# Performance work log

Hardware: AMD Instinct MI355X
Metric: run time of the kernel (lower is better)

The kernel has to match this reference:

```python
import jax, jax.numpy as jnp
import numpy as np

B, C, H, W = 16, 512, 64, 64
HEADS = 8
DIL = 2  # dilation of the 3x3 depthwise conv (padding == dilation -> shape preserving)


def setup_inputs() -> dict:
    key = jax.random.key(0)
    ks = jax.random.split(key, 4)
    x = jax.random.normal(ks[0], (B, C, H, W), jnp.float32)
    # kaiming-normal-ish scales (fan_out, relu)
    w_qkv = jax.random.normal(ks[1], (3 * C, C), jnp.float32) * (2.0 / C) ** 0.5  # 1x1 conv weight
    w_dw = jax.random.normal(ks[2], (C, 3, 3), jnp.float32) * (2.0 / 9.0) ** 0.5  # depthwise 3x3
    w_out = jax.random.normal(ks[3], (C, C), jnp.float32) * (2.0 / C) ** 0.5      # 1x1 conv weight
    temperature = jnp.sqrt(jnp.asarray(C // HEADS, jnp.float32))                  # init sqrt(dim_per_head)
    return {"x": x, "w_qkv": w_qkv, "w_dw": w_dw, "w_out": w_out, "temperature": temperature}


def _dw_conv(y, w_dw):
    # depthwise dilated 3x3 conv, padding=dilation -> same spatial size
    rhs = w_dw[:, None, :, :]  # [C,1,3,3]
    return jax.lax.conv_general_dilated(
        y, rhs, window_strides=(1, 1), padding=((DIL, DIL), (DIL, DIL)),
        rhs_dilation=(DIL, DIL), feature_group_count=y.shape[1],
        dimension_numbers=("NCHW", "OIHW", "NCHW"))


def reference(x, w_qkv, w_dw, w_out, temperature):
    b, c, h, w = x.shape
    n = h * w
    d = c // HEADS
    # 1x1 qkv projection (bias-free conv == einsum)
    qkv = jnp.einsum("oc,bchw->bohw", w_qkv, x)  # [B,3C,H,W]
    q, k, v = jnp.split(qkv, 3, axis=1)
    # same depthwise conv applied to q,k,v: fold into batch, conv once
    qkv3 = _dw_conv(jnp.concatenate([q, k, v], axis=0), w_dw)  # [3B,C,H,W]
    q, k, v = jnp.split(qkv3, 3, axis=0)
    q = q.reshape(b, HEADS, d, n)
    k = k.reshape(b, HEADS, d, n)
    v = v.reshape(b, HEADS, d, n)
    # L2 normalize along the per-head channel dim (dim=2), eps=1e-12 like F.normalize
    l2 = lambda t: t / jnp.maximum(jnp.linalg.norm(t, axis=2, keepdims=True), 1e-12)
    q = l2(q)
    k = l2(k)
    # cross-covariance attention: [B,heads,d,d]
    attn = jnp.einsum("bhdn,bhen->bhde", q, k) / jnp.maximum(temperature, 1e-5)
    attn = jax.nn.softmax(attn, axis=-1)
    # dropout is identity in eval mode
    out = jnp.einsum("bhde,bhen->bhdn", attn, v).reshape(b, c, h, w)
    return jnp.einsum("oc,bchw->bohw", w_out, out)
```

## Files before the change

kernel.cpp:

```cpp
#include <hip/hip_runtime.h>

typedef __attribute__((ext_vector_type(8))) short bf16x8;
typedef __attribute__((ext_vector_type(8))) unsigned short ushort8;
typedef __attribute__((ext_vector_type(4))) float f32x4;
typedef __attribute__((ext_vector_type(4))) unsigned int u32x4;
typedef __attribute__((ext_vector_type(2))) unsigned int u32x2;

__device__ __forceinline__ float bf2f(unsigned short u) {
  union { unsigned int i; float f; } v; v.i = ((unsigned int)u) << 16; return v.f;
}
__device__ __forceinline__ float asf(unsigned int u) {
  union { unsigned int i; float f; } v; v.i = u; return v.f;
}
__device__ __forceinline__ unsigned short f2bf(float f) {
  union { float f; unsigned int i; } v; v.f = f;
  unsigned int u = v.i;
  return (unsigned short)((u + 0x7FFFu + ((u >> 16) & 1u)) >> 16);
}
__device__ __forceinline__ void gload16(const void* g, void* l) {
  __builtin_amdgcn_global_load_lds(
      (const __attribute__((address_space(1))) void*)g,
      (__attribute__((address_space(3))) void*)l, 16, 0, 0);
}

__global__ __launch_bounds__(256) void cvt_f32_bf16(const float* __restrict__ s,
                                                    unsigned short* __restrict__ d, int n) {
  int i = blockIdx.x * 256 + threadIdx.x;
  if (i < n) d[i] = f2bf(s[i]);
}

__global__ __launch_bounds__(256) void transpose_x(const float* __restrict__ x,
                                                   unsigned short* __restrict__ xt) {
  __shared__ float tile[64][65];
  const int b = blockIdx.z, ct = blockIdx.y, nt = blockIdx.x;
  const int t = threadIdx.x;
  const int r0 = t >> 6, col = t & 63;
  const float* src = x + ((size_t)b * 512 + ct * 64) * 4096 + nt * 64;
#pragma unroll
  for (int i = 0; i < 16; ++i) {
    int r = i * 4 + r0;
    tile[r][col] = src[(size_t)r * 4096 + col];
  }
  __syncthreads();
  unsigned short* dst = xt + ((size_t)b * 4096 + nt * 64) * 512 + ct * 64;
#pragma unroll
  for (int i = 0; i < 16; ++i) {
    int n = i * 4 + r0;
    dst[(size_t)n * 512 + col] = f2bf(tile[col][n]);
  }
}

__global__ __launch_bounds__(512, 2) void gemm_qkv_256(const unsigned short* __restrict__ A,
                                                       const unsigned short* __restrict__ B,
                                                       unsigned short* __restrict__ C) {
  __shared__ unsigned short lA[2][256 * 64];
  __shared__ unsigned short lB[2][256 * 64];
  const int gx = gridDim.x;
  const int nwg = gx * gridDim.y;
  int flat = blockIdx.x + gx * blockIdx.y;
  flat = (flat & 7) * (nwg >> 3) + (flat >> 3);
  const int bx = flat % gx;
  const int by = flat / gx;
  const size_t m0 = (size_t)by * 256;
  const size_t n0 = (size_t)bx * 256;

  const int t = threadIdx.x;
  const int lane = t & 63;
  const int wid = t >> 6;
  const int wm = wid >> 2, wn = wid & 3;
  const int ro = lane & 15, kq = lane >> 4;

  const int srow = t >> 3;
  const int kslot = (t & 7) ^ (srow & 7);
  const unsigned short* ga = A + (m0 + srow) * 512 + kslot * 8;
  const unsigned short* gb = B + (n0 + srow) * 512 + kslot * 8;

  f32x4 acc[8][4] = {};

  auto stage = [&](int kt, int bbuf) {
    char* da = (char*)(&lA[bbuf][0]) + t * 16;
    char* db = (char*)(&lB[bbuf][0]) + t * 16;
    const unsigned short* pa = ga + kt * 64;
    const unsigned short* pb = gb + kt * 64;
#pragma unroll
    for (int l = 0; l < 4; ++l) {
      gload16(pa + (size_t)(l * 64) * 512, da + l * 8192);
      gload16(pb + (size_t)(l * 64) * 512, db + l * 8192);
    }
  };

  stage(0, 0);
  __syncthreads();
  int buf = 0;
  for (int kt = 0; kt < 8; ++kt) {
    if (kt + 1 < 8) stage(kt + 1, buf ^ 1);
    const unsigned short* pa = &lA[buf][0];
    const unsigned short* pb = &lB[buf][0];
#pragma unroll
    for (int kk = 0; kk < 2; ++kk) {
      const int slot = ((kk << 2) | kq) ^ (ro & 7);
      bf16x8 a_[8], b_[4];
#pragma unroll
      for (int i = 0; i < 8; ++i) {
        const int row = wm * 128 + i * 16 + ro;
        a_[i] = *(const bf16x8*)&pa[row * 64 + slot * 8];
      }
#pragma unroll
      for (int j = 0; j < 4; ++j) {
        const int row = wn * 64 + j * 16 + ro;
        b_[j] = *(const bf16x8*)&pb[row * 64 + slot * 8];
      }
#pragma unroll
      for (int i = 0; i < 8; ++i)
#pragma unroll
        for (int j = 0; j < 4; ++j)
          acc[i][j] = __builtin_amdgcn_mfma_f32_16x16x32_bf16(a_[i], b_[j], acc[i][j], 0, 0, 0);
    }
    __syncthreads();
    buf ^= 1;
  }

#pragma unroll
  for (int i = 0; i < 8; ++i)
#pragma unroll
    for (int j = 0; j < 4; ++j)
#pragma unroll
      for (int r = 0; r < 4; ++r) {
        size_t row = m0 + wm * 128 + i * 16 + (kq << 2) + r;
        size_t col = n0 + wn * 64 + j * 16 + ro;
        C[row * 1536 + col] = f2bf(acc[i][j][r]);
      }
}

template <bool BF16OUT>
__global__ __launch_bounds__(256) void gemm_bt(const unsigned short* __restrict__ A,
                                               const unsigned short* __restrict__ B,
                                               void* __restrict__ Cv, int K, int ldc,
                                               size_t sA, size_t sB, size_t sC) {
  __shared__ unsigned short lA[2][128 * 32];
  __shared__ unsigned short lB[2][128 * 32];
  const int gx = gridDim.x, gy = gridDim.y;
  const int nwg = gx * gy * gridDim.z;
  int flat = blockIdx.x + gx * (blockIdx.y + gy * blockIdx.z);
  flat = (flat & 7) * (nwg >> 3) + (flat >> 3);
  const int bx = flat % gx;
  const int rem = flat / gx;
  const int by = rem % gy;
  const int bz = rem / gy;

  const int t = threadIdx.x;
  const int lane = t & 63;
  const int wv = t >> 6, wr = wv >> 1, wc = wv & 1;
  const size_t m0 = (size_t)by * 128;
  const size_t n0 = (size_t)bx * 128;
  A += (size_t)bz * sA;
  B += (size_t)bz * sB;
  const unsigned short* ga = A + (m0 + (t >> 2)) * (size_t)K + (t & 3) * 8;
  const unsigned short* gb = B + (n0 + (t >> 2)) * (size_t)K + (t & 3) * 8;
  const size_t gstep = (size_t)64 * K;

  f32x4 acc[4][4] = {};

  auto stage = [&](int kt, int bbuf) {
    const unsigned short* pa = ga + kt * 32;
    const unsigned short* pb = gb + kt * 32;
    char* da = (char*)(&lA[bbuf][0]) + t * 16;
    char* db = (char*)(&lB[bbuf][0]) + t * 16;
    gload16(pa, da);
    gload16(pa + gstep, da + 4096);
    gload16(pb, db);
    gload16(pb + gstep, db + 4096);
  };

  const int nk = K >> 5;
  stage(0, 0);
  __syncthreads();
  int buf = 0;
  for (int kt = 0; kt < nk; ++kt) {
    if (kt + 1 < nk) stage(kt + 1, buf ^ 1);
    const unsigned short* pa = &lA[buf][0];
    const unsigned short* pb = &lB[buf][0];
    const int ro = lane & 15, ko = (lane >> 4) * 8;
    bf16x8 af[4], bv[4];
#pragma unroll
    for (int i = 0; i < 4; ++i) af[i] = *(const bf16x8*)&pa[(wr * 64 + i * 16 + ro) * 32 + ko];
#pragma unroll
    for (int i = 0; i < 4; ++i) bv[i] = *(const bf16x8*)&pb[(wc * 64 + i * 16 + ro) * 32 + ko];
#pragma unroll
    for (int i = 0; i < 4; ++i)
#pragma unroll
      for (int j = 0; j < 4; ++j)
        acc[i][j] = __builtin_amdgcn_mfma_f32_16x16x32_bf16(af[i], bv[j], acc[i][j], 0, 0, 0);
    __syncthreads();
    buf ^= 1;
  }

  if constexpr (BF16OUT) {
    unsigned short* C = (unsigned short*)Cv + (size_t)bz * sC;
#pragma unroll
    for (int i = 0; i < 4; ++i)
#pragma unroll
      for (int j = 0; j < 4; ++j)
#pragma unroll
        for (int r = 0; r < 4; ++r) {
          size_t row = m0 + wr * 64 + i * 16 + ((lane >> 4) << 2) + r;
          size_t col = n0 + wc * 64 + j * 16 + (lane & 15);
          C[row * (size_t)ldc + col] = f2bf(acc[i][j][r]);
        }
  } else {
    float* C = (float*)Cv + (size_t)bz * sC;
#pragma unroll
    for (int i = 0; i < 4; ++i)
#pragma unroll
      for (int j = 0; j < 4; ++j)
#pragma unroll
        for (int r = 0; r < 4; ++r) {
          size_t row = m0 + wr * 64 + i * 16 + ((lane >> 4) << 2) + r;
          size_t col = n0 + wc * 64 + j * 16 + (lane & 15);
          C[row * (size_t)ldc + col] = acc[i][j][r];
        }
  }
}

struct Row3h { u32x2 v[3]; };

__global__ __launch_bounds__(256) void dwconv_norm(const unsigned short* __restrict__ Y,
                                                   const float* __restrict__ wdw,
                                                   unsigned short* __restrict__ Qb,
                                                   unsigned short* __restrict__ Kb,
                                                   unsigned short* __restrict__ Vb) {
  const int t = threadIdx.x, lane = t & 63, wv = t >> 6;
  const int bid = blockIdx.x;
  const int lbid = (bid & 7) * 384 + (bid >> 3);
  const int wid = lbid * 4 + wv;
  const int sub = wid & 3;
  const int x = (wid >> 2) & 63;
  const int grp = wid >> 8;
  const int par = sub >> 1, chhalf = sub & 1;
  const int b = grp / 3, part = grp - b * 3;
  const int c0 = chhalf * 256 + (lane >> 4) * 64 + (lane & 15) * 4;

  float wr[36];
  const float* wp = wdw + c0 * 9;
#pragma unroll
  for (int i = 0; i < 9; ++i) {
    f32x4 q = *(const f32x4*)(wp + i * 4);
    wr[i * 4 + 0] = q[0]; wr[i * 4 + 1] = q[1];
    wr[i * 4 + 2] = q[2]; wr[i * 4 + 3] = q[3];
  }

  const size_t ybase = (size_t)b * 4096 * 1536 + part * 512 + c0;
  const bool okm = (x >= 2), okp = (x <= 61);
  const int xm = okm ? x - 2 : x;
  const int xp = okp ? x + 2 : x;

  auto loadrow = [&](int yy) -> Row3h {
    Row3h r;
    const bool oky = ((unsigned)yy < 64u);
    const int yyc = oky ? yy : 0;
    const size_t rb = ybase + (size_t)(yyc * 64) * 1536;
    u32x2 a = *(const u32x2*)(Y + rb + (size_t)xm * 1536);
    u32x2 c = *(const u32x2*)(Y + rb + (size_t)x * 1536);
    u32x2 d = *(const u32x2*)(Y + rb + (size_t)xp * 1536);
    r.v[0] = a & ((oky && okm) ? 0xFFFFFFFFu : 0u);
    r.v[1] = c & (oky ? 0xFFFFFFFFu : 0u);
    r.v[2] = d & ((oky && okp) ? 0xFFFFFFFFu : 0u);
    return r;
  };

  Row3h W[3];
#pragma unroll
  for (int xt = 0; xt < 3; ++xt) W[0].v[xt] = (u32x2)(0u);
  W[1] = loadrow(par);
  W[2] = loadrow(par + 2);

  unsigned short* dst0 = (part == 0 ? Qb : (part == 1 ? Kb : Vb)) +
                         ((size_t)b * 4096 + x) * 512 + c0;

#pragma unroll
  for (int i = 0; i < 32; ++i) {
    const int y = par + 2 * i;
    float acc[4] = {0.f, 0.f, 0.f, 0.f};
#pragma unroll
    for (int r = 0; r < 3; ++r) {
      const Row3h& R = W[(i + r) % 3];
#pragma unroll
      for (int xt = 0; xt < 3; ++xt) {
        const int tap = r * 3 + xt;
        const u32x2 v = R.v[xt];
#pragma unroll
        for (int m = 0; m < 2; ++m) {
          const unsigned int w2 = v[m];
          acc[2 * m]     += asf(w2 << 16)         * wr[(2 * m) * 9 + tap];
          acc[2 * m + 1] += asf(w2 & 0xFFFF0000u) * wr[(2 * m + 1) * 9 + tap];
        }
      }
    }
    if (part < 2) {
      float ss = 0.f;
#pragma unroll
      for (int j = 0; j < 4; ++j) ss += acc[j] * acc[j];
      ss += __shfl_xor(ss, 1);
      ss += __shfl_xor(ss, 2);
      ss += __shfl_xor(ss, 4);
      ss += __shfl_xor(ss, 8);
      const float rcp = 1.f / fmaxf(sqrtf(ss), 1e-12f);
#pragma unroll
      for (int j = 0; j < 4; ++j) acc[j] *= rcp;
    }
    u32x2 pk;
    pk[0] = (unsigned int)f2bf(acc[0]) | ((unsigned int)f2bf(acc[1]) << 16);
    pk[1] = (unsigned int)f2bf(acc[2]) | ((unsigned int)f2bf(acc[3]) << 16);
    *(u32x2*)(dst0 + (size_t)y * 64 * 512) = pk;
    if (i < 31) W[i % 3] = loadrow(y + 4);
  }
}

__global__ __launch_bounds__(256) void attn_partial(const unsigned short* __restrict__ Qb,
                                                    const unsigned short* __restrict__ Kb,
                                                    float* __restrict__ Spart) {
  __shared__ unsigned short sQ[4][64][72];
  __shared__ unsigned short sK[4][64][72];
  const int t = threadIdx.x, lane = t & 63, wv = t >> 6;
  const int bh = blockIdx.x >> 2;
  const int s = (blockIdx.x & 3) * 4 + wv;
  const int b = bh >> 3, h = bh & 7;
  const unsigned short* qbase = Qb + ((size_t)b * 4096) * 512 + h * 64;
  const unsigned short* kbase = Kb + ((size_t)b * 4096) * 512 + h * 64;
  f32x4 acc[4][4] = {};
  for (int ch = 0; ch < 4; ++ch) {
    const int n0 = s * 256 + ch * 64;
    const unsigned short* qp = qbase + (size_t)(n0 + lane) * 512;
    const unsigned short* kp = kbase + (size_t)(n0 + lane) * 512;
    ushort8 qv[8], kv[8];
#pragma unroll
    for (int v = 0; v < 8; ++v) qv[v] = *(const ushort8*)(qp + v * 8);
#pragma unroll
    for (int v = 0; v < 8; ++v) kv[v] = *(const ushort8*)(kp + v * 8);
#pragma unroll
    for (int v = 0; v < 8; ++v)
#pragma unroll
      for (int j = 0; j < 8; ++j) {
        sQ[wv][v * 8 + j][lane] = qv[v][j];
        sK[wv][v * 8 + j][lane] = kv[v][j];
      }
    __syncthreads();
    const int ro = lane & 15, ko = (lane >> 4) * 8;
#pragma unroll
    for (int ks = 0; ks < 2; ++ks) {
      bf16x8 af[4], bv[4];
#pragma unroll
      for (int i = 0; i < 4; ++i) af[i] = *(const bf16x8*)&sQ[wv][i * 16 + ro][ks * 32 + ko];
#pragma unroll
      for (int i = 0; i < 4; ++i) bv[i] = *(const bf16x8*)&sK[wv][i * 16 + ro][ks * 32 + ko];
#pragma unroll
      for (int i = 0; i < 4; ++i)
#pragma unroll
        for (int j = 0; j < 4; ++j)
          acc[i][j] = __builtin_amdgcn_mfma_f32_16x16x32_bf16(af[i], bv[j], acc[i][j], 0, 0, 0);
    }
    __syncthreads();
  }
  float* dst = Spart + ((size_t)bh * 16 + s) * 4096;
#pragma unroll
  for (int i = 0; i < 4; ++i)
#pragma unroll
    for (int j = 0; j < 4; ++j)
#pragma unroll
      for (int r = 0; r < 4; ++r) {
        int d = i * 16 + ((lane >> 4) << 2) + r;
        int e = j * 16 + (lane & 15);
        dst[d * 64 + e] = acc[i][j][r];
      }
}

__global__ __launch_bounds__(256) void softmax_attn(const float* __restrict__ Spart,
                                                    const float* __restrict__ tptr,
                                                    unsigned short* __restrict__ attn) {
  const int bh = blockIdx.x, t = threadIdx.x;
  const int d = t >> 2, eb = (t & 3) << 4;
  const float inv_t = 1.f / fmaxf(tptr[0], 1e-5f);
  float v[16];
#pragma unroll
  for (int i = 0; i < 16; ++i) v[i] = 0.f;
  for (int s = 0; s < 16; ++s) {
    const f32x4* p = (const f32x4*)(Spart + ((size_t)bh * 16 + s) * 4096 + d * 64 + eb);
#pragma unroll
    for (int i = 0; i < 4; ++i) {
      f32x4 q = p[i];
      v[i * 4 + 0] += q[0]; v[i * 4 + 1] += q[1];
      v[i * 4 + 2] += q[2]; v[i * 4 + 3] += q[3];
    }
  }
  float mx = -1e30f;
#pragma unroll
  for (int i = 0; i < 16; ++i) { v[i] *= inv_t; mx = fmaxf(mx, v[i]); }
  mx = fmaxf(mx, __shfl_xor(mx, 1));
  mx = fmaxf(mx, __shfl_xor(mx, 2));
  float sm = 0.f;
#pragma unroll
  for (int i = 0; i < 16; ++i) { v[i] = __expf(v[i] - mx); sm += v[i]; }
  sm += __shfl_xor(sm, 1);
  sm += __shfl_xor(sm, 2);
  const float r = 1.f / sm;
  ushort8 pk0, pk1;
#pragma unroll
  for (int i = 0; i < 8; ++i) { pk0[i] = f2bf(v[i] * r); pk1[i] = f2bf(v[8 + i] * r); }
  ushort8* dst = (ushort8*)(attn + (size_t)bh * 4096 + d * 64 + eb);
  dst[0] = pk0; dst[1] = pk1;
}

__global__ __launch_bounds__(256) void make_w2(const unsigned short* __restrict__ attn,
                                               const float* __restrict__ w_out,
                                               unsigned short* __restrict__ w2) {
  __shared__ float sA[4096];
  const int bx = blockIdx.x;
  const int bh = bx >> 1, half = bx & 1;
  const int b = bh >> 3, h = bh & 7;
  const int t = threadIdx.x;
  for (int i = t; i < 4096; i += 256) sA[i] = bf2f(attn[(size_t)bh * 4096 + i]);
  __syncthreads();
  const int o = half * 256 + t;
  float w[64];
  const float* wp = w_out + (size_t)o * 512 + h * 64;
#pragma unroll
  for (int i = 0; i < 64; i += 4) {
    f32x4 q = *(const f32x4*)(wp + i);
    w[i] = q[0]; w[i + 1] = q[1]; w[i + 2] = q[2]; w[i + 3] = q[3];
  }
  unsigned short* dst = w2 + ((size_t)b * 512 + o) * 512 + h * 64;
#pragma unroll 1
  for (int eg = 0; eg < 8; ++eg) {
    ushort8 pk;
#pragma unroll
    for (int ee = 0; ee < 8; ++ee) {
      const int e = eg * 8 + ee;
      float acc = 0.f;
#pragma unroll
      for (int dd = 0; dd < 64; ++dd) acc += w[dd] * sA[dd * 64 + e];
      pk[ee] = f2bf(acc);
    }
    *(ushort8*)(dst + eg * 8) = pk;
  }
}

extern "C" void kernel_launch(void* const* d_in, const int* in_sizes, int n_in,
                              void* d_out, int out_size, void* d_ws, size_t ws_size,
                              hipStream_t stream) {
  const float* x     = (const float*)d_in[0];
  const float* w_qkv = (const float*)d_in[1];
  const float* w_dw  = (const float*)d_in[2];
  const float* w_out = (const float*)d_in[3];
  const float* temp  = (const float*)d_in[4];
  float* out = (float*)d_out;

  char* ws = (char*)d_ws;
  const size_t MB = 1024 * 1024;
  unsigned short* Xt    = (unsigned short*)(ws);
  float*          Spart = (float*)(ws);
  unsigned short* attn  = (unsigned short*)(ws + 32 * MB);
  unsigned short* w2    = (unsigned short*)(ws + 33 * MB);
  unsigned short* Y     = (unsigned short*)(ws + 64 * MB);
  unsigned short* Qb    = (unsigned short*)(ws + 256 * MB);
  unsigned short* Kb    = (unsigned short*)(ws + 320 * MB);
  unsigned short* Vb    = (unsigned short*)(ws + 384 * MB);
  unsigned short* Wq    = (unsigned short*)(ws + 448 * MB);

  cvt_f32_bf16<<<3072, 256, 0, stream>>>(w_qkv, Wq, 1536 * 512);
  transpose_x<<<dim3(64, 8, 16), 256, 0, stream>>>(x, Xt);
  gemm_qkv_256<<<dim3(6, 256), 512, 0, stream>>>(Xt, Wq, Y);
  dwconv_norm<<<3072, 256, 0, stream>>>(Y, w_dw, Qb, Kb, Vb);
  attn_partial<<<512, 256, 0, stream>>>(Qb, Kb, Spart);
  softmax_attn<<<128, 256, 0, stream>>>(Spart, temp, attn);
  make_w2<<<256, 256, 0, stream>>>(attn, w_out, w2);
  gemm_bt<false><<<dim3(32, 4, 16), 256, 0, stream>>>(
      w2, Vb, out, 512, 4096,
      (size_t)512 * 512, (size_t)4096 * 512, (size_t)512 * 4096);
}
```

Baseline: 418.8 us.

## Restructure QKV GEMM main loop into phased pipeline with split staging

Rewrites the QKV projection GEMM inner loop into four sub-phases per K tile, each separated by barriers. A and B tile loads are staged in halves interleaved with MFMA groups, using explicit vmcnt waits and s_setprio around MFMA bursts, and A is prefetched two tiles ahead. The aim is to hide global-to-LDS load latency behind compute and cut register pressure; launch bounds drop to one block per CU. The cost is more barriers and reliance on hand-tuned waitcnt counts that must match the number of outstanding loads.

After: 438.9 us. 4.8% more time.

```diff
diff --git a/kernel.cpp b/kernel.cpp
--- a/kernel.cpp
+++ b/kernel.cpp
@@ -50,7 +50,7 @@
   }
 }
 
-__global__ __launch_bounds__(512, 2) void gemm_qkv_256(const unsigned short* __restrict__ A,
+__global__ __launch_bounds__(512, 1) void gemm_qkv_8ph(const unsigned short* __restrict__ A,
                                                        const unsigned short* __restrict__ B,
                                                        unsigned short* __restrict__ C) {
   __shared__ unsigned short lA[2][256 * 64];
@@ -71,53 +71,94 @@
   const int ro = lane & 15, kq = lane >> 4;
 
   const int srow = t >> 3;
-  const int kslot = (t & 7) ^ (srow & 7);
-  const unsigned short* ga = A + (m0 + srow) * 512 + kslot * 8;
-  const unsigned short* gb = B + (n0 + srow) * 512 + kslot * 8;
+  const int sslot = t & 7;
+  const int kslot = sslot ^ (srow & 7);
+
+  auto stageA = [&](int kt, int h, int bbuf) {
+    char* d = (char*)(&lA[bbuf][0]) + ((h * 128 + srow) * 64 + sslot * 8) * 2;
+    const unsigned short* g = A + (m0 + h * 128 + srow) * 512 + kt * 64 + kslot * 8;
+    gload16(g, d);
+    gload16(g + (size_t)64 * 512, d + 64 * 128);
+  };
+  auto stageB = [&](int kt, int h, int bbuf) {
+    char* d = (char*)(&lB[bbuf][0]) + ((h * 128 + srow) * 64 + sslot * 8) * 2;
+    const unsigned short* g = B + (n0 + h * 128 + srow) * 512 + kt * 64 + kslot * 8;
+    gload16(g, d);
+    gload16(g + (size_t)64 * 512, d + 64 * 128);
+  };
 
   f32x4 acc[8][4] = {};
 
-  auto stage = [&](int kt, int bbuf) {
-    char* da = (char*)(&lA[bbuf][0]) + t * 16;
-    char* db = (char*)(&lB[bbuf][0]) + t * 16;
-    const unsigned short* pa = ga + kt * 64;
-    const unsigned short* pb = gb + kt * 64;
-#pragma unroll
-    for (int l = 0; l < 4; ++l) {
-      gload16(pa + (size_t)(l * 64) * 512, da + l * 8192);
-      gload16(pb + (size_t)(l * 64) * 512, db + l * 8192);
-    }
-  };
-
-  stage(0, 0);
-  __syncthreads();
-  int buf = 0;
+  stageA(0, 0, 0); stageA(0, 1, 0);
+  stageB(0, 0, 0); stageB(0, 1, 0);
+  stageA(1, 0, 1); stageA(1, 1, 1);
+
+#pragma unroll 1
   for (int kt = 0; kt < 8; ++kt) {
-    if (kt + 1 < 8) stage(kt + 1, buf ^ 1);
-    const unsigned short* pa = &lA[buf][0];
-    const unsigned short* pb = &lB[buf][0];
-#pragma unroll
-    for (int kk = 0; kk < 2; ++kk) {
-      const int slot = ((kk << 2) | kq) ^ (ro & 7);
-      bf16x8 a_[8], b_[4];
-#pragma unroll
-      for (int i = 0; i < 8; ++i) {
-        const int row = wm * 128 + i * 16 + ro;
-        a_[i] = *(const bf16x8*)&pa[row * 64 + slot * 8];
-      }
-#pragma unroll
-      for (int j = 0; j < 4; ++j) {
-        const int row = wn * 64 + j * 16 + ro;
-        b_[j] = *(const bf16x8*)&pb[row * 64 + slot * 8];
-      }
-#pragma unroll
-      for (int i = 0; i < 8; ++i)
-#pragma unroll
-        for (int j = 0; j < 4; ++j)
-          acc[i][j] = __builtin_amdgcn_mfma_f32_16x16x32_bf16(a_[i], b_[j], acc[i][j], 0, 0, 0);
-    }
-    __syncthreads();
-    buf ^= 1;
+    const int c = kt & 1;
+    if (kt == 7) { asm volatile("s_waitcnt vmcnt(0)" ::: "memory"); }
+    else         { asm volatile("s_waitcnt vmcnt(4)" ::: "memory"); }
+    __builtin_amdgcn_s_barrier();
+    asm volatile("" ::: "memory");
+    const unsigned short* pa = &lA[c][0];
+    const unsigned short* pb = &lB[c][0];
+    const int slot0 = kq ^ (ro & 7);
+    const int slot1 = (4 + kq) ^ (ro & 7);
+
+    if (kt + 1 < 8) stageB(kt + 1, 0, c ^ 1);
+    bf16x8 a0[8], bv0, bv1;
+#pragma unroll
+    for (int i = 0; i < 8; ++i)
+      a0[i] = *(const bf16x8*)&pa[(wm * 128 + i * 16 + ro) * 64 + slot0 * 8];
+    bv0 = *(const bf16x8*)&pb[(wn * 64 + 0 * 16 + ro) * 64 + slot0 * 8];
+    bv1 = *(const bf16x8*)&pb[(wn * 64 + 1 * 16 + ro) * 64 + slot0 * 8];
+    __builtin_amdgcn_s_setprio(1);
+#pragma unroll
+    for (int i = 0; i < 8; ++i) {
+      acc[i][0] = __builtin_amdgcn_mfma_f32_16x16x32_bf16(a0[i], bv0, acc[i][0], 0, 0, 0);
+      acc[i][1] = __builtin_amdgcn_mfma_f32_16x16x32_bf16(a0[i], bv1, acc[i][1], 0, 0, 0);
+    }
+    __builtin_amdgcn_s_setprio(0);
+    __builtin_amdgcn_s_barrier();
+
+    if (kt + 1 < 8) stageB(kt + 1, 1, c ^ 1);
+    bv0 = *(const bf16x8*)&pb[(wn * 64 + 2 * 16 + ro) * 64 + slot0 * 8];
+    bv1 = *(const bf16x8*)&pb[(wn * 64 + 3 * 16 + ro) * 64 + slot0 * 8];
+    __builtin_amdgcn_s_setprio(1);
+#pragma unroll
+    for (int i = 0; i < 8; ++i) {
+      acc[i][2] = __builtin_amdgcn_mfma_f32_16x16x32_bf16(a0[i], bv0, acc[i][2], 0, 0, 0);
+      acc[i][3] = __builtin_amdgcn_mfma_f32_16x16x32_bf16(a0[i], bv1, acc[i][3], 0, 0, 0);
+    }
+    __builtin_amdgcn_s_setprio(0);
+    __builtin_amdgcn_s_barrier();
+
+    bf16x8 a1[8];
+#pragma unroll
+    for (int i = 0; i < 8; ++i)
+      a1[i] = *(const bf16x8*)&pa[(wm * 128 + i * 16 + ro) * 64 + slot1 * 8];
+    bv0 = *(const bf16x8*)&pb[(wn * 64 + 0 * 16 + ro) * 64 + slot1 * 8];
+    bv1 = *(const bf16x8*)&pb[(wn * 64 + 1 * 16 + ro) * 64 + slot1 * 8];
+    __builtin_amdgcn_s_setprio(1);
+#pragma unroll
+    for (int i = 0; i < 8; ++i) {
+      acc[i][0] = __builtin_amdgcn_mfma_f32_16x16x32_bf16(a1[i], bv0, acc[i][0], 0, 0, 0);
+      acc[i][1] = __builtin_amdgcn_mfma_f32_16x16x32_bf16(a1[i], bv1, acc[i][1], 0, 0, 0);
+    }
+    __builtin_amdgcn_s_setprio(0);
+    asm volatile("s_waitcnt lgkmcnt(0)" ::: "memory");
+    __builtin_amdgcn_s_barrier();
+
+    if (kt + 2 < 8) { stageA(kt + 2, 0, c); stageA(kt + 2, 1, c); }
+    bv0 = *(const bf16x8*)&pb[(wn * 64 + 2 * 16 + ro) * 64 + slot1 * 8];
+    bv1 = *(const bf16x8*)&pb[(wn * 64 + 3 * 16 + ro) * 64 + slot1 * 8];
+    __builtin_amdgcn_s_setprio(1);
+#pragma unroll
+    for (int i = 0; i < 8; ++i) {
+      acc[i][2] = __builtin_amdgcn_mfma_f32_16x16x32_bf16(a1[i], bv0, acc[i][2], 0, 0, 0);
+      acc[i][3] = __builtin_amdgcn_mfma_f32_16x16x32_bf16(a1[i], bv1, acc[i][3], 0, 0, 0);
+    }
+    __builtin_amdgcn_s_setprio(0);
   }
 
 #pragma unroll
@@ -468,7 +509,7 @@
 
   cvt_f32_bf16<<<3072, 256, 0, stream>>>(w_qkv, Wq, 1536 * 512);
   transpose_x<<<dim3(64, 8, 16), 256, 0, stream>>>(x, Xt);
-  gemm_qkv_256<<<dim3(6, 256), 512, 0, stream>>>(Xt, Wq, Y);
+  gemm_qkv_8ph<<<dim3(6, 256), 512, 0, stream>>>(Xt, Wq, Y);
   dwconv_norm<<<3072, 256, 0, stream>>>(Y, w_dw, Qb, Kb, Vb);
   attn_partial<<<512, 256, 0, stream>>>(Qb, Kb, Spart);
   softmax_attn<<<128, 256, 0, stream>>>(Spart, temp, attn);
```
